# Kernel tuning notes

Measured on AMD Instinct MI355X. Metric: run time of the kernel, lower is better.

The kernel has to match this reference:

```python
import jax, jax.numpy as jnp
import numpy as np

RADIUS = 0.2
MAX_SAMPLES = 9  # matches Conv2d kernel_size=[1, 9]


def ball_query(pcs, radius, nsample):
    """pcs: [B, 3, N] -> group_idx: [B, N, nsample] int32.
    First index of each group is the center point itself (distance 0)."""
    p = jnp.transpose(pcs, (0, 2, 1))  # [B, N, 3]
    sq = jnp.sum(p * p, axis=-1)  # [B, N]
    # pairwise squared distances [B, N, N]
    d2 = sq[:, :, None] + sq[:, None, :] - 2.0 * jnp.einsum('bnd,bmd->bnm', p, p)
    B, N, _ = d2.shape
    idx = jnp.broadcast_to(jnp.arange(N, dtype=jnp.int32), (B, N, N))
    idx = jnp.where(d2 > radius * radius, N, idx)  # out-of-ball -> sentinel N
    idx = jnp.sort(idx, axis=-1)[:, :, :nsample]  # in-ball indices first (ascending)
    first = idx[:, :, 0:1]  # center index (self, d2=0)
    idx = jnp.where(idx == N, first, idx)  # pad with center
    return idx


def setup_inputs() -> dict:
    key = jax.random.key(0)
    k1, k2, k3 = jax.random.split(key, 3)
    B, C_in, C_out, N = 4, 64, 128, 4096
    x = jax.random.normal(k1, (B, C_in, N), dtype=jnp.float32)
    pcs = jax.random.uniform(k2, (B, 3, N), dtype=jnp.float32)
    # Conv2d(in, out, [1, 9]) weight, xavier_uniform; bias zero-init
    fan_in = C_in * 1 * MAX_SAMPLES
    fan_out = C_out * 1 * MAX_SAMPLES
    limit = float(np.sqrt(6.0 / (fan_in + fan_out)))
    W = jax.random.uniform(k3, (C_out, C_in, MAX_SAMPLES), dtype=jnp.float32,
                           minval=-limit, maxval=limit)
    b = jnp.zeros((C_out,), dtype=jnp.float32)
    return {"x": x, "pcs": pcs, "W": W, "b": b}


def reference(x, pcs, W, b):
    """x: [B, C_in, N], pcs: [B, 3, N], W: [C_out, C_in, 9], b: [C_out].
    Returns y: [B, C_out, N]."""
    idx = ball_query(pcs, RADIUS, MAX_SAMPLES)  # [B, N, S]
    # gather grouped features: [B, C_in, N, S]
    x_grp = jnp.take_along_axis(x[:, :, None, :], idx[:, None, :, :], axis=3)
    # grouped, center-normalized coordinates (as in _group_points)
    pcs_grp = jnp.take_along_axis(pcs[:, :, None, :], idx[:, None, :, :], axis=3)
    pcs_grp = pcs_grp - pcs[:, :, :, None]  # [B, 3, N, S] (computed for fidelity)
    # Conv2d(in, out, [1, 9]) over [B, C_in, N, S] -> [B, C_out, N]
    y = jnp.einsum('bcns,ocs->bon', x_grp, W) + b[None, :, None]
    return y
```

## Files before the change

### kernel.cpp

```cpp
#include <hip/hip_runtime.h>

#define N_PTS 4096
#define B_SZ 4
#define C_IN 64
#define C_OUT 128
#define NS 9
#define KTOT (C_IN * NS)
#define RAD2 0.04f

typedef __attribute__((ext_vector_type(8))) short bf16x8;
typedef __attribute__((ext_vector_type(4))) float f32x4;

__device__ inline ushort f2bf(float f) {
    union { float f; unsigned u; } v; v.f = f;
    unsigned r = (v.u + 0x7FFF + ((v.u >> 16) & 1)) >> 16;
    return (ushort)r;
}

__device__ inline void gl_lds16(const void* g, void* l) {
    __builtin_amdgcn_global_load_lds(
        (const __attribute__((address_space(1))) unsigned int*)g,
        (__attribute__((address_space(3))) unsigned int*)l, 16, 0, 0);
}

#define LOADG4(gi, qx, qy, qz) do {                                         \
    int base_ = (gi) * 256 + 4 * lane;                                      \
    qx = *(const float4*)(pb + base_);                                      \
    qy = *(const float4*)(pb + N_PTS + base_);                              \
    qz = *(const float4*)(pb + 2 * N_PTS + base_);                          \
} while (0)

#define PROCG4(gi, qx, qy, qz) do {                                         \
    unsigned long long mm_[4]; int hit_[4];                                 \
    const float* fx_ = (const float*)&qx;                                   \
    const float* fy_ = (const float*)&qy;                                   \
    const float* fz_ = (const float*)&qz;                                   \
    _Pragma("unroll")                                                       \
    for (int k_ = 0; k_ < 4; ++k_) {                                        \
        float X_ = fx_[k_], Y_ = fy_[k_], Z_ = fz_[k_];                     \
        float sqm_ = __fadd_rn(__fadd_rn(__fmul_rn(X_, X_),                 \
                                         __fmul_rn(Y_, Y_)),               \
                               __fmul_rn(Z_, Z_));                          \
        float dot_ = __fadd_rn(__fadd_rn(__fmul_rn(cx, X_),                 \
                                         __fmul_rn(cy, Y_)),               \
                               __fmul_rn(cz, Z_));                          \
        float d2_ = __fsub_rn(__fadd_rn(csq, sqm_), __fmul_rn(2.0f, dot_)); \
        hit_[k_] = !(d2_ > RAD2);                                           \
        mm_[k_] = __ballot(hit_[k_]);                                       \
    }                                                                       \
    unsigned long long any_ = mm_[0] | mm_[1] | mm_[2] | mm_[3];            \
    if (any_) {                                                             \
        if (first < 0) {                                                    \
            int f_ = 0x7fffffff;                                            \
            _Pragma("unroll")                                               \
            for (int k_ = 0; k_ < 4; ++k_)                                  \
                if (mm_[k_]) {                                              \
                    int i_ = (gi) * 256 + 4 * (__ffsll(mm_[k_]) - 1) + k_;  \
                    f_ = min(f_, i_);                                       \
                }                                                           \
            first = f_;                                                     \
        }                                                                   \
        int p_ = 0;                                                         \
        _Pragma("unroll")                                                   \
        for (int k_ = 0; k_ < 4; ++k_)                                      \
            p_ += __builtin_amdgcn_mbcnt_hi((unsigned)(mm_[k_] >> 32),      \
                      __builtin_amdgcn_mbcnt_lo((unsigned)mm_[k_], 0));     \
        int own_ = 0;                                                       \
        _Pragma("unroll")                                                   \
        for (int k_ = 0; k_ < 4; ++k_) {                                    \
            if (hit_[k_]) {                                                 \
                int slot_ = cnt + p_ + own_;                                \
                if (slot_ < NS)                                             \
                    outb[(size_t)slot_ * N_PTS] = (gi) * 256 + 4 * lane + k_; \
            }                                                               \
            own_ += hit_[k_];                                               \
        }                                                                   \
        cnt += __popcll(mm_[0]) + __popcll(mm_[1])                          \
             + __popcll(mm_[2]) + __popcll(mm_[3]);                         \
    }                                                                       \
} while (0)

__global__ void __launch_bounds__(256) prep_kernel(
    const float* __restrict__ W, const float* __restrict__ x,
    const float* __restrict__ pcs,
    ushort* __restrict__ Wt, ushort* __restrict__ xT, int* __restrict__ idxT)
{
    __shared__ ushort tile[64][66];
    const int t = threadIdx.x;
    const int blk = blockIdx.x;

    if (blk < 4096) {
        const int lane = t & 63;
        const int pt = t >> 6;
        const int widp = blk * 4 + pt;
        const int b = widp >> 12;
        const int n = widp & (N_PTS - 1);
        const float* pb = pcs + (size_t)b * 3 * N_PTS;
        float cx = pb[n], cy = pb[N_PTS + n], cz = pb[2 * N_PTS + n];
        float csq = __fadd_rn(__fadd_rn(__fmul_rn(cx, cx), __fmul_rn(cy, cy)),
                              __fmul_rn(cz, cz));
        int* outb = idxT + (size_t)b * NS * N_PTS + n;
        int cnt = 0, first = -1;
        float4 ax, ay, az, bx, by, bz;
        LOADG4(0, ax, ay, az);
        #pragma unroll 1
        for (int g = 0; g < 16; g += 2) {
            if (g + 1 < 16) LOADG4(g + 1, bx, by, bz);
            PROCG4(g, ax, ay, az);
            if (cnt >= NS) break;
            if (g + 2 < 16) LOADG4(g + 2, ax, ay, az);
            PROCG4(g + 1, bx, by, bz);
            if (cnt >= NS) break;
        }
        if (lane >= cnt && lane < NS) outb[(size_t)lane * N_PTS] = first;
    } else if (blk < 4384) {
        int id = (blk - 4096) * 256 + t;
        int o = id / KTOT;
        int r = id - o * KTOT;
        int s = r >> 6, c = r & 63;
        int dst = o * KTOT + s * 64 + (((c >> 3) ^ (o & 7)) << 3) + (c & 7);
        Wt[dst] = f2bf(W[o * KTOT + c * NS + s]);
    } else {
        int r = blk - 4384;
        int b = r >> 6;
        int n0 = (r & 63) * 64;
        const float* xb = x + (size_t)b * C_IN * N_PTS;
        #pragma unroll
        for (int i = 0; i < 16; ++i) {
            int flat = i * 256 + t;
            int c = flat >> 6, n = flat & 63;
            tile[c][n] = f2bf(xb[(size_t)c * N_PTS + n0 + n]);
        }
        __syncthreads();
        ushort* xTb = xT + ((size_t)b * N_PTS + n0) * C_IN;
        #pragma unroll
        for (int i = 0; i < 16; ++i) {
            int flat = i * 256 + t;
            int n = flat >> 6, c = flat & 63;
            xTb[(size_t)n * C_IN + c] = tile[c][n];
        }
    }
}

__global__ void __launch_bounds__(512) conv_kernel(
    const ushort* __restrict__ xT, const ushort* __restrict__ Wt,
    const int* __restrict__ idxT, const float* __restrict__ bias,
    float* __restrict__ y)
{
    __shared__ __align__(16) ushort Wlds[64 * KTOT];
    __shared__ __align__(16) ushort Xlds[576 * 64];

    const int t = threadIdx.x;
    const int lane = t & 63;
    const int wid = t >> 6;
    const int ntile = blockIdx.x;
    const int b = blockIdx.y;
    const int n64 = ntile * 64;
    const int l15 = lane & 15;
    const int l4 = lane >> 4;

    const ushort* xTb = xT + (size_t)b * N_PTS * C_IN;
    const int* idxTb = idxT + (size_t)b * NS * N_PTS;

    const int rb = wid * 72;
    int g[9];
    #pragma unroll
    for (int j = 0; j < 9; ++j) {
        int r = rb + j * 8 + (lane >> 3);
        g[j] = idxTb[((r >> 6) << 12) + n64 + (r & 63)];
    }

    #pragma unroll
    for (int j = 0; j < 9; ++j) {
        int off = (wid * 9 + j) * 512 + lane * 8;
        gl_lds16(Wt + off, &Wlds[off]);
    }
    {
        const int sx = (((lane & 7) ^ (lane >> 3)) << 3);
        #pragma unroll
        for (int j = 0; j < 9; ++j)
            gl_lds16(xTb + ((size_t)g[j] << 6) + sx,
                     &Xlds[(rb + j * 8) * 64 + lane * 8]);
    }
    __syncthreads();

    const int m0 = (wid & 1) * 32;
    const int n0w = (wid >> 1) * 16;
    const int ra0 = m0 + l15;
    const int rb0 = n0w + l15;
    const int swA = ra0 & 7;
    const int swB = rb0 & 7;
    float* yb = y + (size_t)b * C_OUT * N_PTS + n64;

    #pragma unroll
    for (int half = 0; half < 2; ++half) {
        f32x4 acc[2];
        acc[0] = (f32x4){0.f, 0.f, 0.f, 0.f};
        acc[1] = (f32x4){0.f, 0.f, 0.f, 0.f};

        #pragma unroll
        for (int s = 0; s < NS; ++s) {
            #pragma unroll
            for (int hh = 0; hh < 2; ++hh) {
                int d = hh * 4 + l4;
                bf16x8 a0 = *(const bf16x8*)&Wlds[ra0 * KTOT + s * 64 + ((d ^ swA) << 3)];
                bf16x8 a1 = *(const bf16x8*)&Wlds[(ra0 + 16) * KTOT + s * 64 + ((d ^ swA) << 3)];
                bf16x8 b0 = *(const bf16x8*)&Xlds[(s * 64 + rb0) * 64 + ((d ^ swB) << 3)];
                acc[0] = __builtin_amdgcn_mfma_f32_16x16x32_bf16(a0, b0, acc[0], 0, 0, 0);
                acc[1] = __builtin_amdgcn_mfma_f32_16x16x32_bf16(a1, b0, acc[1], 0, 0, 0);
            }
        }

        #pragma unroll
        for (int fm = 0; fm < 2; ++fm) {
            #pragma unroll
            for (int j = 0; j < 4; ++j) {
                int o = half * 64 + m0 + fm * 16 + l4 * 4 + j;
                yb[(size_t)o * N_PTS + n0w + l15] = acc[fm][j] + bias[o];
            }
        }

        if (half == 0) {
            __syncthreads();
            #pragma unroll
            for (int j = 0; j < 9; ++j) {
                int off = (wid * 9 + j) * 512 + lane * 8;
                gl_lds16(Wt + 36864 + off, &Wlds[off]);
            }
            __syncthreads();
        }
    }
}

extern "C" void kernel_launch(void* const* d_in, const int* in_sizes, int n_in,
                              void* d_out, int out_size, void* d_ws, size_t ws_size,
                              hipStream_t stream) {
    const float* x    = (const float*)d_in[0];
    const float* pcs  = (const float*)d_in[1];
    const float* W    = (const float*)d_in[2];
    const float* bias = (const float*)d_in[3];
    float* y = (float*)d_out;

    int*    idxT = (int*)d_ws;
    ushort* xT   = (ushort*)((char*)d_ws + 851968);
    ushort* Wt   = (ushort*)((char*)d_ws + 2949120);

    prep_kernel<<<4640, 256, 0, stream>>>(W, x, pcs, Wt, xT, idxT);
    conv_kernel<<<dim3(64, B_SZ), 512, 0, stream>>>(xT, Wt, idxT, bias, y);
}
```

Before: 20.82 us.

## Process four ball-query centers per wavefront to reuse loaded candidate points

Each wavefront now handles four query centers instead of one, so each candidate-point load and its squared norm are shared across four centers. The grid shrinks accordingly, and the weight and x transpose blocks are moved to the front of the block range so they are scheduled first. In exchange, a wavefront keeps scanning until all four centers have nine neighbours, so its early exit comes later, and register use goes up.

```diff
diff --git a/kernel.cpp b/kernel.cpp
--- a/kernel.cpp
+++ b/kernel.cpp
@@ -30,55 +30,66 @@
     qz = *(const float4*)(pb + 2 * N_PTS + base_);                          \
 } while (0)
 
-#define PROCG4(gi, qx, qy, qz) do {                                         \
-    unsigned long long mm_[4]; int hit_[4];                                 \
+#define PROCG5(gi, qx, qy, qz) do {                                         \
     const float* fx_ = (const float*)&qx;                                   \
     const float* fy_ = (const float*)&qy;                                   \
     const float* fz_ = (const float*)&qz;                                   \
+    float sqm_[4];                                                          \
     _Pragma("unroll")                                                       \
-    for (int k_ = 0; k_ < 4; ++k_) {                                        \
-        float X_ = fx_[k_], Y_ = fy_[k_], Z_ = fz_[k_];                     \
-        float sqm_ = __fadd_rn(__fadd_rn(__fmul_rn(X_, X_),                 \
-                                         __fmul_rn(Y_, Y_)),               \
-                               __fmul_rn(Z_, Z_));                          \
-        float dot_ = __fadd_rn(__fadd_rn(__fmul_rn(cx, X_),                 \
-                                         __fmul_rn(cy, Y_)),               \
-                               __fmul_rn(cz, Z_));                          \
-        float d2_ = __fsub_rn(__fadd_rn(csq, sqm_), __fmul_rn(2.0f, dot_)); \
-        hit_[k_] = !(d2_ > RAD2);                                           \
-        mm_[k_] = __ballot(hit_[k_]);                                       \
-    }                                                                       \
-    unsigned long long any_ = mm_[0] | mm_[1] | mm_[2] | mm_[3];            \
-    if (any_) {                                                             \
-        if (first < 0) {                                                    \
-            int f_ = 0x7fffffff;                                            \
+    for (int k_ = 0; k_ < 4; ++k_)                                          \
+        sqm_[k_] = __fadd_rn(__fadd_rn(__fmul_rn(fx_[k_], fx_[k_]),         \
+                                       __fmul_rn(fy_[k_], fy_[k_])),        \
+                             __fmul_rn(fz_[k_], fz_[k_]));                  \
+    _Pragma("unroll")                                                       \
+    for (int c_ = 0; c_ < 4; ++c_) {                                        \
+        if (cnt[c_] < NS) {                                                 \
+            unsigned long long mm_[4]; int hit_[4];                         \
             _Pragma("unroll")                                               \
-            for (int k_ = 0; k_ < 4; ++k_)                                  \
-                if (mm_[k_]) {                                              \
-                    int i_ = (gi) * 256 + 4 * (__ffsll(mm_[k_]) - 1) + k_;  \
-                    f_ = min(f_, i_);                                       \
+            for (int k_ = 0; k_ < 4; ++k_) {                                \
+                float dot_ = __fadd_rn(__fadd_rn(__fmul_rn(cx[c_], fx_[k_]),\
+                                                 __fmul_rn(cy[c_], fy_[k_])),\
+                                       __fmul_rn(cz[c_], fz_[k_]));         \
+                float d2_ = __fsub_rn(__fadd_rn(csq[c_], sqm_[k_]),         \
+                                      __fmul_rn(2.0f, dot_));               \
+                hit_[k_] = !(d2_ > RAD2);                                   \
+                mm_[k_] = __ballot(hit_[k_]);                               \
+            }                                                               \
+            unsigned long long any_ = mm_[0] | mm_[1] | mm_[2] | mm_[3];    \
+            if (any_) {                                                     \
+                if (first[c_] < 0) {                                        \
+                    int f_ = 0x7fffffff;                                    \
+                    _Pragma("unroll")                                       \
+                    for (int k_ = 0; k_ < 4; ++k_)                          \
+                        if (mm_[k_]) {                                      \
+                            int i_ = (gi) * 256 + 4 * (__ffsll(mm_[k_]) - 1) + k_; \
+                            f_ = min(f_, i_);                               \
+                        }                                                   \
+                    first[c_] = f_;                                         \
                 }                                                           \
-            first = f_;                                                     \
+                int p_ = 0;                                                 \
+                _Pragma("unroll")                                           \
+                for (int k_ = 0; k_ < 4; ++k_)                              \
+                    p_ += __builtin_amdgcn_mbcnt_hi((unsigned)(mm_[k_] >> 32), \
+                              __builtin_amdgcn_mbcnt_lo((unsigned)mm_[k_], 0)); \
+                int own_ = 0;                                               \
+                _Pragma("unroll")                                           \
+                for (int k_ = 0; k_ < 4; ++k_) {                            \
+                    if (hit_[k_]) {                                         \
+                        int slot_ = cnt[c_] + p_ + own_;                    \
+                        if (slot_ < NS)                                     \
+                            outB[(size_t)slot_ * N_PTS + c_] =              \
+                                (gi) * 256 + 4 * lane + k_;                 \
+                    }                                                       \
+                    own_ += hit_[k_];                                       \
+                }                                                           \
+                cnt[c_] += __popcll(mm_[0]) + __popcll(mm_[1])              \
+                         + __popcll(mm_[2]) + __popcll(mm_[3]);             \
+            }                                                               \
         }                                                                   \
-        int p_ = 0;                                                         \
-        _Pragma("unroll")                                                   \
-        for (int k_ = 0; k_ < 4; ++k_)                                      \
-            p_ += __builtin_amdgcn_mbcnt_hi((unsigned)(mm_[k_] >> 32),      \
-                      __builtin_amdgcn_mbcnt_lo((unsigned)mm_[k_], 0));     \
-        int own_ = 0;                                                       \
-        _Pragma("unroll")                                                   \
-        for (int k_ = 0; k_ < 4; ++k_) {                                    \
-            if (hit_[k_]) {                                                 \
-                int slot_ = cnt + p_ + own_;                                \
-                if (slot_ < NS)                                             \
-                    outb[(size_t)slot_ * N_PTS] = (gi) * 256 + 4 * lane + k_; \
-            }                                                               \
-            own_ += hit_[k_];                                               \
-        }                                                                   \
-        cnt += __popcll(mm_[0]) + __popcll(mm_[1])                          \
-             + __popcll(mm_[2]) + __popcll(mm_[3]);                         \
     }                                                                       \
 } while (0)
+
+#define ALLDONE (cnt[0] >= NS && cnt[1] >= NS && cnt[2] >= NS && cnt[3] >= NS)
 
 __global__ void __launch_bounds__(256) prep_kernel(
     const float* __restrict__ W, const float* __restrict__ x,
@@ -89,56 +100,68 @@
     const int t = threadIdx.x;
     const int blk = blockIdx.x;
 
-    if (blk < 4096) {
+    if (blk < 288) {
+        int id = blk * 256 + t;
+        int o = id / KTOT;
+        int r = id - o * KTOT;
+        int s = r >> 6, c = r & 63;
+        int dst = o * KTOT + s * 64 + (((c >> 3) ^ (o & 7)) << 3) + (c & 7);
+        Wt[dst] = f2bf(W[o * KTOT + c * NS + s]);
+    } else if (blk < 544) {
+        int r = blk - 288;
+        int b = r >> 6;
+        int n0 = (r & 63) * 64;
+        const float* xb = x + (size_t)b * C_IN * N_PTS;
+        #pragma unroll
+        for (int i = 0; i < 16; ++i) {
+            int flat = i * 256 + t;
+            int c = flat >> 6, n = flat & 63;
+            tile[c][n] = f2bf(xb[(size_t)c * N_PTS + n0 + n]);
+        }
+        __syncthreads();
+        ushort* xTb = xT + ((size_t)b * N_PTS + n0) * C_IN;
+        #pragma unroll
+        for (int i = 0; i < 16; ++i) {
+            int flat = i * 256 + t;
+            int n = flat >> 6, c = flat & 63;
+            xTb[(size_t)n * C_IN + c] = tile[c][n];
+        }
+    } else {
         const int lane = t & 63;
-        const int pt = t >> 6;
-        const int widp = blk * 4 + pt;
-        const int b = widp >> 12;
-        const int n = widp & (N_PTS - 1);
+        const int wid = t >> 6;
+        const int nb16 = (blk - 544) * 16 + wid * 4;
+        const int b = nb16 >> 12;
+        const int n0 = nb16 & (N_PTS - 1);
         const float* pb = pcs + (size_t)b * 3 * N_PTS;
-        float cx = pb[n], cy = pb[N_PTS + n], cz = pb[2 * N_PTS + n];
-        float csq = __fadd_rn(__fadd_rn(__fmul_rn(cx, cx), __fmul_rn(cy, cy)),
-                              __fmul_rn(cz, cz));
-        int* outb = idxT + (size_t)b * NS * N_PTS + n;
-        int cnt = 0, first = -1;
+
+        float cx[4], cy[4], cz[4], csq[4];
+        #pragma unroll
+        for (int c = 0; c < 4; ++c) {
+            int n = n0 + c;
+            cx[c] = pb[n]; cy[c] = pb[N_PTS + n]; cz[c] = pb[2 * N_PTS + n];
+            csq[c] = __fadd_rn(__fadd_rn(__fmul_rn(cx[c], cx[c]),
+                                         __fmul_rn(cy[c], cy[c])),
+                               __fmul_rn(cz[c], cz[c]));
+        }
+        int* outB = idxT + (size_t)b * NS * N_PTS + n0;
+        int cnt[4] = {0, 0, 0, 0};
+        int first[4] = {-1, -1, -1, -1};
+
         float4 ax, ay, az, bx, by, bz;
         LOADG4(0, ax, ay, az);
         #pragma unroll 1
         for (int g = 0; g < 16; g += 2) {
             if (g + 1 < 16) LOADG4(g + 1, bx, by, bz);
-            PROCG4(g, ax, ay, az);
-            if (cnt >= NS) break;
+            PROCG5(g, ax, ay, az);
+            if (ALLDONE) break;
             if (g + 2 < 16) LOADG4(g + 2, ax, ay, az);
-            PROCG4(g + 1, bx, by, bz);
-            if (cnt >= NS) break;
-        }
-        if (lane >= cnt && lane < NS) outb[(size_t)lane * N_PTS] = first;
-    } else if (blk < 4384) {
-        int id = (blk - 4096) * 256 + t;
-        int o = id / KTOT;
-        int r = id - o * KTOT;
-        int s = r >> 6, c = r & 63;
-        int dst = o * KTOT + s * 64 + (((c >> 3) ^ (o & 7)) << 3) + (c & 7);
-        Wt[dst] = f2bf(W[o * KTOT + c * NS + s]);
-    } else {
-        int r = blk - 4384;
-        int b = r >> 6;
-        int n0 = (r & 63) * 64;
-        const float* xb = x + (size_t)b * C_IN * N_PTS;
-        #pragma unroll
-        for (int i = 0; i < 16; ++i) {
-            int flat = i * 256 + t;
-            int c = flat >> 6, n = flat & 63;
-            tile[c][n] = f2bf(xb[(size_t)c * N_PTS + n0 + n]);
-        }
-        __syncthreads();
-        ushort* xTb = xT + ((size_t)b * N_PTS + n0) * C_IN;
-        #pragma unroll
-        for (int i = 0; i < 16; ++i) {
-            int flat = i * 256 + t;
-            int n = flat >> 6, c = flat & 63;
-            xTb[(size_t)n * C_IN + c] = tile[c][n];
-        }
+            PROCG5(g + 1, bx, by, bz);
+            if (ALLDONE) break;
+        }
+        #pragma unroll
+        for (int c = 0; c < 4; ++c)
+            if (lane >= cnt[c] && lane < NS)
+                outB[(size_t)lane * N_PTS + c] = first[c];
     }
 }
 
@@ -245,6 +268,6 @@
     ushort* xT   = (ushort*)((char*)d_ws + 851968);
     ushort* Wt   = (ushort*)((char*)d_ws + 2949120);
 
-    prep_kernel<<<4640, 256, 0, stream>>>(W, x, pcs, Wt, xT, idxT);
+    prep_kernel<<<1568, 256, 0, stream>>>(W, x, pcs, Wt, xT, idxT);
     conv_kernel<<<dim3(64, B_SZ), 512, 0, stream>>>(xT, Wt, idxT, bias, y);
 }
```

New measurement: 21.00 us. Within noise of the previous version (+0.9%).
